# Kernel optimization log

Hardware: AMD Instinct MI355X
Metric: run time of the kernel (lower is better)

The kernel has to match this reference:

```python
import jax, jax.numpy as jnp
import numpy as np

GAIN_CAP = 0.99
EPS = 1e-4


def _clamp(v):
    # clamp_preserve_grad(v, 0.0, cap) == cap - relu(cap - relu(v))
    r = jax.nn.relu
    return GAIN_CAP - r(GAIN_CAP - r(v))


def _pos(p):
    return jax.nn.softplus(p) + EPS


def setup_inputs() -> dict:
    key = jax.random.key(0)
    ks = jax.random.split(key, 12)
    B, C, H, W, O, M = 4, 128, 256, 256, 16, 32
    return {
        "x": jax.random.normal(ks[0], (B, C, H, W), jnp.float32),
        "steer": jax.random.normal(ks[1], (B, O, H, W), jnp.float32),
        "modulation": jax.random.normal(ks[2], (B, M), jnp.float32),
        "r_center": 0.1 * jax.random.normal(ks[3], (C,), jnp.float32),
        "r_horizontal": 0.1 * jax.random.normal(ks[4], (C,), jnp.float32),
        "r_vertical": 0.1 * jax.random.normal(ks[5], (C,), jnp.float32),
        "r_diag": 0.1 * jax.random.normal(ks[6], (C,), jnp.float32),
        "gain_horizontal": 0.1 * jax.random.normal(ks[7], (C,), jnp.float32),
        "gain_vertical": 0.1 * jax.random.normal(ks[8], (C,), jnp.float32),
        "gain_diag": 0.1 * jax.random.normal(ks[9], (C,), jnp.float32),
        "steer_w": 0.1 * jax.random.normal(ks[10], (4, O), jnp.float32),  # 1x1 conv weight squeezed
        "mod_w": 0.1 * jax.random.normal(ks[11], (3, M), jnp.float32),    # Linear(M,3,bias=False)
    }


def reference(x, steer, modulation, r_center, r_horizontal, r_vertical, r_diag,
              gain_horizontal, gain_vertical, gain_diag, steer_w, mod_w):
    cview = lambda p: p[None, :, None, None]  # (1,C,1,1)
    center = x
    right = jnp.roll(x, -1, axis=-1)
    left = jnp.roll(x, 1, axis=-1)
    up = jnp.roll(x, 1, axis=-2)
    down = jnp.roll(x, -1, axis=-2)
    diag_ne = jnp.roll(x, (-1, -1), axis=(-2, -1))
    diag_sw = jnp.roll(x, (1, 1), axis=(-2, -1))
    diag_nw = jnp.roll(x, (1, -1), axis=(-2, -1))
    diag_se = jnp.roll(x, (-1, 1), axis=(-2, -1))

    r_c = cview(_pos(r_center))
    r_h = cview(_pos(r_horizontal))
    r_v = cview(_pos(r_vertical))
    r_d = cview(_pos(r_diag))

    flow_h = (right - center + (left - center)) / (r_c + r_h)
    flow_v = (up - center + (down - center)) / (r_c + r_v)
    flow_d = (diag_ne - center + (diag_sw - center) + (diag_nw - center) + (diag_se - center)) / (2.0 * (r_c + r_d))

    gh = jnp.tanh(cview(gain_horizontal))
    gv = jnp.tanh(cview(gain_vertical))
    gd = jnp.tanh(cview(gain_diag))

    # modulation gating: [B,3] -> [B,3,1,1]
    delta = jnp.tanh(modulation @ mod_w.T)[:, :, None, None]
    gh = _clamp(gh * (1.0 + 0.1 * delta[:, 0:1]))
    gv = _clamp(gv * (1.0 + 0.1 * delta[:, 1:2]))
    gd = _clamp(gd * (1.0 + 0.1 * delta[:, 2:3]))

    # steer gating: 1x1 conv (no bias) then tanh -> [B,4,H,W]
    steer_fields = jnp.tanh(jnp.einsum('bohw,po->bphw', steer, steer_w))
    gh = _clamp(gh * (1.0 + 0.2 * steer_fields[:, 0:1]))
    gv = _clamp(gv * (1.0 + 0.2 * steer_fields[:, 1:2]))
    gd = _clamp(gd * (1.0 + 0.2 * steer_fields[:, 2:3]))

    update = gh * flow_h + gv * flow_v + gd * flow_d
    return center + update
```

## Files before the change

kernel.cpp:

```cpp
#include <hip/hip_runtime.h>
#include <math.h>

#define GAIN_CAP 0.99f
#define EPSV 1e-4f

static constexpr int B = 4, C = 128, H = 256, W = 256, O = 16, M = 32;
static constexpr int HW = H * W;

static constexpr int SF_SZ = B * 3 * HW;
static constexpr int G_SZ  = B * C * 3;

__device__ __forceinline__ float softplusf(float x) {
    return log1pf(expf(-fabsf(x))) + fmaxf(x, 0.0f);
}
__device__ __forceinline__ float clampg(float v) {
    return fminf(fmaxf(v, 0.0f), GAIN_CAP);
}

__global__ void setup_kernel(const float* __restrict__ r_center,
                             const float* __restrict__ r_h,
                             const float* __restrict__ r_v,
                             const float* __restrict__ r_d,
                             const float* __restrict__ g_h,
                             const float* __restrict__ g_v,
                             const float* __restrict__ g_d,
                             const float* __restrict__ modulation,
                             const float* __restrict__ mod_w,
                             float* __restrict__ gains,
                             float* __restrict__ invd)
{
    int t = threadIdx.x;
    int b = t >> 7;
    int c = t & (C - 1);

    float rc = softplusf(r_center[c]) + EPSV;
    float dh = rc + softplusf(r_h[c]) + EPSV;
    float dv = rc + softplusf(r_v[c]) + EPSV;
    float dd = 2.0f * (rc + softplusf(r_d[c]) + EPSV);
    if (b == 0) {
        invd[c * 3 + 0] = 1.0f / dh;
        invd[c * 3 + 1] = 1.0f / dv;
        invd[c * 3 + 2] = 1.0f / dd;
    }

    float a0 = 0.f, a1 = 0.f, a2 = 0.f;
#pragma unroll
    for (int m = 0; m < M; ++m) {
        float mv = modulation[b * M + m];
        a0 += mv * mod_w[0 * M + m];
        a1 += mv * mod_w[1 * M + m];
        a2 += mv * mod_w[2 * M + m];
    }
    float d0 = tanhf(a0), d1 = tanhf(a1), d2 = tanhf(a2);

    gains[(b * C + c) * 3 + 0] = clampg(tanhf(g_h[c]) * (1.0f + 0.1f * d0));
    gains[(b * C + c) * 3 + 1] = clampg(tanhf(g_v[c]) * (1.0f + 0.1f * d1));
    gains[(b * C + c) * 3 + 2] = clampg(tanhf(g_d[c]) * (1.0f + 0.1f * d2));
}

__global__ void steer_kernel(const float* __restrict__ steer,
                             const float* __restrict__ steer_w,
                             float* __restrict__ sf)
{
    int idx = blockIdx.x * blockDim.x + threadIdx.x;
    int b  = idx >> 16;
    int hw = idx & (HW - 1);

    const float* sp = steer + (size_t)b * O * HW + hw;
    float a0 = 0.f, a1 = 0.f, a2 = 0.f;
#pragma unroll
    for (int o = 0; o < O; ++o) {
        float v = sp[(size_t)o * HW];
        a0 += v * steer_w[0 * O + o];
        a1 += v * steer_w[1 * O + o];
        a2 += v * steer_w[2 * O + o];
    }
    sf[(size_t)(b * 3 + 0) * HW + hw] = tanhf(a0);
    sf[(size_t)(b * 3 + 1) * HW + hw] = tanhf(a1);
    sf[(size_t)(b * 3 + 2) * HW + hw] = tanhf(a2);
}

__global__ void __launch_bounds__(256)
main_kernel(const float* __restrict__ x,
            const float* __restrict__ sf,
            const float* __restrict__ gains,
            const float* __restrict__ invd,
            float* __restrict__ out)
{
    int idx = blockIdx.x * 256 + threadIdx.x;
    int w  = idx & (W - 1);
    int h  = (idx >> 8) & (H - 1);
    int bc = idx >> 16;
    int c  = bc & (C - 1);
    int b  = bc >> 7;

    const float* plane = x + (size_t)bc * HW;
    int wp = (w + 1) & (W - 1), wm = (w - 1) & (W - 1);
    int hp = (h + 1) & (H - 1), hm = (h - 1) & (H - 1);
    const float* row_c = plane + h  * W;
    const float* row_u = plane + hm * W;
    const float* row_d = plane + hp * W;

    float center = row_c[w];
    float right  = row_c[wp], left = row_c[wm];
    float up     = row_u[w],  down = row_d[w];
    float ne = row_d[wp], sw = row_u[wm], nw = row_u[wp], se = row_d[wm];

    float fh = (right + left - 2.0f * center) * invd[c * 3 + 0];
    float fv = (up + down - 2.0f * center)    * invd[c * 3 + 1];
    float fd = (ne + sw + nw + se - 4.0f * center) * invd[c * 3 + 2];

    int hw = (h << 8) | w;
    float s0 = sf[(size_t)(b * 3 + 0) * HW + hw];
    float s1 = sf[(size_t)(b * 3 + 1) * HW + hw];
    float s2 = sf[(size_t)(b * 3 + 2) * HW + hw];

    float gh = clampg(gains[bc * 3 + 0] * (1.0f + 0.2f * s0));
    float gv = clampg(gains[bc * 3 + 1] * (1.0f + 0.2f * s1));
    float gd = clampg(gains[bc * 3 + 2] * (1.0f + 0.2f * s2));

    out[idx] = center + gh * fh + gv * fv + gd * fd;
}

extern "C" void kernel_launch(void* const* d_in, const int* in_sizes, int n_in,
                              void* d_out, int out_size, void* d_ws, size_t ws_size,
                              hipStream_t stream) {
    const float* x          = (const float*)d_in[0];
    const float* steer      = (const float*)d_in[1];
    const float* modulation = (const float*)d_in[2];
    const float* r_center   = (const float*)d_in[3];
    const float* r_horiz    = (const float*)d_in[4];
    const float* r_vert     = (const float*)d_in[5];
    const float* r_diag     = (const float*)d_in[6];
    const float* g_horiz    = (const float*)d_in[7];
    const float* g_vert     = (const float*)d_in[8];
    const float* g_diag     = (const float*)d_in[9];
    const float* steer_w    = (const float*)d_in[10];
    const float* mod_w      = (const float*)d_in[11];

    float* ws    = (float*)d_ws;
    float* sf    = ws;
    float* gains = ws + SF_SZ;
    float* invd  = gains + G_SZ;
    float* out   = (float*)d_out;

    setup_kernel<<<1, B * C, 0, stream>>>(r_center, r_horiz, r_vert, r_diag,
                                          g_horiz, g_vert, g_diag,
                                          modulation, mod_w, gains, invd);
    steer_kernel<<<(B * HW) / 256, 256, 0, stream>>>(steer, steer_w, sf);
    main_kernel<<<(B * C * HW) / 256, 256, 0, stream>>>(x, sf, gains, invd, out);
}
```

Baseline: 339.0 us.

## Row-streaming stencil with float4 loads, wave shuffles, and fused setup kernel

The main kernel now has each wavefront walk a strip of 16 rows of one plane. It loads each row once as float4 and keeps the up, center and down rows in registers, so vertical neighbours are reused across iterations. Horizontal neighbours come from cross-lane shuffles, and output goes out through non-temporal vector stores. The setup work is folded into the steer kernel, which is also vectorized to float4, removing one launch. The cost is fewer blocks, less parallelism and serial dependence along rows.

```diff
diff --git a/kernel.cpp b/kernel.cpp
--- a/kernel.cpp
+++ b/kernel.cpp
@@ -6,6 +6,8 @@
 
 static constexpr int B = 4, C = 128, H = 256, W = 256, O = 16, M = 32;
 static constexpr int HW = H * W;
+
+typedef float vfloat4 __attribute__((ext_vector_type(4)));
 
 static constexpr int SF_SZ = B * 3 * HW;
 static constexpr int G_SZ  = B * C * 3;
@@ -17,67 +19,64 @@
     return fminf(fmaxf(v, 0.0f), GAIN_CAP);
 }
 
-__global__ void setup_kernel(const float* __restrict__ r_center,
-                             const float* __restrict__ r_h,
-                             const float* __restrict__ r_v,
-                             const float* __restrict__ r_d,
-                             const float* __restrict__ g_h,
-                             const float* __restrict__ g_v,
-                             const float* __restrict__ g_d,
-                             const float* __restrict__ modulation,
-                             const float* __restrict__ mod_w,
-                             float* __restrict__ gains,
-                             float* __restrict__ invd)
+__global__ void __launch_bounds__(256)
+steer_kernel(const float* __restrict__ steer,
+             const float* __restrict__ steer_w,
+             const float* __restrict__ r_center,
+             const float* __restrict__ r_h,
+             const float* __restrict__ r_v,
+             const float* __restrict__ r_d,
+             const float* __restrict__ g_h,
+             const float* __restrict__ g_v,
+             const float* __restrict__ g_d,
+             const float* __restrict__ modulation,
+             const float* __restrict__ mod_w,
+             float* __restrict__ sf,
+             float* __restrict__ gains,
+             float* __restrict__ invd)
 {
-    int t = threadIdx.x;
-    int b = t >> 7;
-    int c = t & (C - 1);
-
-    float rc = softplusf(r_center[c]) + EPSV;
-    float dh = rc + softplusf(r_h[c]) + EPSV;
-    float dv = rc + softplusf(r_v[c]) + EPSV;
-    float dd = 2.0f * (rc + softplusf(r_d[c]) + EPSV);
-    if (b == 0) {
-        invd[c * 3 + 0] = 1.0f / dh;
-        invd[c * 3 + 1] = 1.0f / dv;
-        invd[c * 3 + 2] = 1.0f / dd;
+    if (blockIdx.x == 0 && threadIdx.x < C) {
+        int c = threadIdx.x;
+        float rc = softplusf(r_center[c]) + EPSV;
+        invd[c * 3 + 0] = 1.0f / (rc + softplusf(r_h[c]) + EPSV);
+        invd[c * 3 + 1] = 1.0f / (rc + softplusf(r_v[c]) + EPSV);
+        invd[c * 3 + 2] = 1.0f / (2.0f * (rc + softplusf(r_d[c]) + EPSV));
+        float th = tanhf(g_h[c]), tv = tanhf(g_v[c]), td = tanhf(g_d[c]);
+        for (int b = 0; b < B; ++b) {
+            float a0 = 0.f, a1 = 0.f, a2 = 0.f;
+#pragma unroll
+            for (int m = 0; m < M; ++m) {
+                float mv = modulation[b * M + m];
+                a0 += mv * mod_w[0 * M + m];
+                a1 += mv * mod_w[1 * M + m];
+                a2 += mv * mod_w[2 * M + m];
+            }
+            gains[(b * C + c) * 3 + 0] = clampg(th * (1.0f + 0.1f * tanhf(a0)));
+            gains[(b * C + c) * 3 + 1] = clampg(tv * (1.0f + 0.1f * tanhf(a1)));
+            gains[(b * C + c) * 3 + 2] = clampg(td * (1.0f + 0.1f * tanhf(a2)));
+        }
     }
 
-    float a0 = 0.f, a1 = 0.f, a2 = 0.f;
-#pragma unroll
-    for (int m = 0; m < M; ++m) {
-        float mv = modulation[b * M + m];
-        a0 += mv * mod_w[0 * M + m];
-        a1 += mv * mod_w[1 * M + m];
-        a2 += mv * mod_w[2 * M + m];
-    }
-    float d0 = tanhf(a0), d1 = tanhf(a1), d2 = tanhf(a2);
+    int idx = blockIdx.x * 256 + threadIdx.x;
+    int b   = idx >> 14;
+    int hw4 = idx & 16383;
+    const float4* sp = (const float4*)(steer + ((size_t)b * O << 16)) + hw4;
 
-    gains[(b * C + c) * 3 + 0] = clampg(tanhf(g_h[c]) * (1.0f + 0.1f * d0));
-    gains[(b * C + c) * 3 + 1] = clampg(tanhf(g_v[c]) * (1.0f + 0.1f * d1));
-    gains[(b * C + c) * 3 + 2] = clampg(tanhf(g_d[c]) * (1.0f + 0.1f * d2));
-}
-
-__global__ void steer_kernel(const float* __restrict__ steer,
-                             const float* __restrict__ steer_w,
-                             float* __restrict__ sf)
-{
-    int idx = blockIdx.x * blockDim.x + threadIdx.x;
-    int b  = idx >> 16;
-    int hw = idx & (HW - 1);
-
-    const float* sp = steer + (size_t)b * O * HW + hw;
-    float a0 = 0.f, a1 = 0.f, a2 = 0.f;
+    float4 a0 = {0,0,0,0}, a1 = {0,0,0,0}, a2 = {0,0,0,0};
 #pragma unroll
     for (int o = 0; o < O; ++o) {
-        float v = sp[(size_t)o * HW];
-        a0 += v * steer_w[0 * O + o];
-        a1 += v * steer_w[1 * O + o];
-        a2 += v * steer_w[2 * O + o];
+        float4 v = sp[(size_t)o << 14];
+        float w0 = steer_w[o], w1 = steer_w[O + o], w2 = steer_w[2 * O + o];
+        a0.x += v.x * w0; a0.y += v.y * w0; a0.z += v.z * w0; a0.w += v.w * w0;
+        a1.x += v.x * w1; a1.y += v.y * w1; a1.z += v.z * w1; a1.w += v.w * w1;
+        a2.x += v.x * w2; a2.y += v.y * w2; a2.z += v.z * w2; a2.w += v.w * w2;
     }
-    sf[(size_t)(b * 3 + 0) * HW + hw] = tanhf(a0);
-    sf[(size_t)(b * 3 + 1) * HW + hw] = tanhf(a1);
-    sf[(size_t)(b * 3 + 2) * HW + hw] = tanhf(a2);
+    float4* o0 = (float4*)(sf + ((size_t)(b * 3 + 0) << 16)) + hw4;
+    float4* o1 = (float4*)(sf + ((size_t)(b * 3 + 1) << 16)) + hw4;
+    float4* o2 = (float4*)(sf + ((size_t)(b * 3 + 2) << 16)) + hw4;
+    *o0 = make_float4(tanhf(a0.x), tanhf(a0.y), tanhf(a0.z), tanhf(a0.w));
+    *o1 = make_float4(tanhf(a1.x), tanhf(a1.y), tanhf(a1.z), tanhf(a1.w));
+    *o2 = make_float4(tanhf(a2.x), tanhf(a2.y), tanhf(a2.z), tanhf(a2.w));
 }
 
 __global__ void __launch_bounds__(256)
@@ -87,39 +86,70 @@
             const float* __restrict__ invd,
             float* __restrict__ out)
 {
-    int idx = blockIdx.x * 256 + threadIdx.x;
-    int w  = idx & (W - 1);
-    int h  = (idx >> 8) & (H - 1);
-    int bc = idx >> 16;
-    int c  = bc & (C - 1);
-    int b  = bc >> 7;
+    constexpr int RPW = 16;
+    int lane  = threadIdx.x & 63;
+    int wave  = threadIdx.x >> 6;
+    int strip = blockIdx.x & 3;
+    int bc    = blockIdx.x >> 2;
+    int c     = bc & (C - 1);
+    int b     = bc >> 7;
+    int h0    = strip * 64 + wave * RPW;
 
-    const float* plane = x + (size_t)bc * HW;
-    int wp = (w + 1) & (W - 1), wm = (w - 1) & (W - 1);
-    int hp = (h + 1) & (H - 1), hm = (h - 1) & (H - 1);
-    const float* row_c = plane + h  * W;
-    const float* row_u = plane + hm * W;
-    const float* row_d = plane + hp * W;
+    const float* plane = x + ((size_t)bc << 16);
+    const float* sfb0  = sf + ((size_t)(b * 3 + 0) << 16);
+    const float* sfb1  = sf + ((size_t)(b * 3 + 1) << 16);
+    const float* sfb2  = sf + ((size_t)(b * 3 + 2) << 16);
+    float*       outp  = out + ((size_t)bc << 16);
 
-    float center = row_c[w];
-    float right  = row_c[wp], left = row_c[wm];
-    float up     = row_u[w],  down = row_d[w];
-    float ne = row_d[wp], sw = row_u[wm], nw = row_u[wp], se = row_d[wm];
+    float ih  = invd[c * 3 + 0], iv = invd[c * 3 + 1], idg = invd[c * 3 + 2];
+    float g0  = gains[bc * 3 + 0], g1 = gains[bc * 3 + 1], g2 = gains[bc * 3 + 2];
 
-    float fh = (right + left - 2.0f * center) * invd[c * 3 + 0];
-    float fv = (up + down - 2.0f * center)    * invd[c * 3 + 1];
-    float fd = (ne + sw + nw + se - 4.0f * center) * invd[c * 3 + 2];
+    int lp = (lane + 1) & 63, lm = (lane - 1) & 63;
 
-    int hw = (h << 8) | w;
-    float s0 = sf[(size_t)(b * 3 + 0) * HW + hw];
-    float s1 = sf[(size_t)(b * 3 + 1) * HW + hw];
-    float s2 = sf[(size_t)(b * 3 + 2) * HW + hw];
+    float4 u4 = ((const float4*)(plane + (((h0 - 1) & 255) << 8)))[lane];
+    float4 c4 = ((const float4*)(plane + (h0 << 8)))[lane];
+    float uRe = __shfl(u4.x, lp), uLe = __shfl(u4.w, lm);
+    float cRe = __shfl(c4.x, lp), cLe = __shfl(c4.w, lm);
 
-    float gh = clampg(gains[bc * 3 + 0] * (1.0f + 0.2f * s0));
-    float gv = clampg(gains[bc * 3 + 1] * (1.0f + 0.2f * s1));
-    float gd = clampg(gains[bc * 3 + 2] * (1.0f + 0.2f * s2));
+    for (int r = 0; r < RPW; ++r) {
+        int h  = h0 + r;
+        int hd = (h + 1) & 255;
+        float4 d4 = ((const float4*)(plane + (hd << 8)))[lane];
+        float4 s0 = ((const float4*)(sfb0 + (h << 8)))[lane];
+        float4 s1 = ((const float4*)(sfb1 + (h << 8)))[lane];
+        float4 s2 = ((const float4*)(sfb2 + (h << 8)))[lane];
+        float dRe = __shfl(d4.x, lp), dLe = __shfl(d4.w, lm);
 
-    out[idx] = center + gh * fh + gv * fv + gd * fd;
+        float cA[4]  = {c4.x, c4.y, c4.z, c4.w};
+        float uA[4]  = {u4.x, u4.y, u4.z, u4.w};
+        float dA[4]  = {d4.x, d4.y, d4.z, d4.w};
+        float crA[4] = {c4.y, c4.z, c4.w, cRe};
+        float clA[4] = {cLe, c4.x, c4.y, c4.z};
+        float urA[4] = {u4.y, u4.z, u4.w, uRe};
+        float ulA[4] = {uLe, u4.x, u4.y, u4.z};
+        float drA[4] = {d4.y, d4.z, d4.w, dRe};
+        float dlA[4] = {dLe, d4.x, d4.y, d4.z};
+        float sA0[4] = {s0.x, s0.y, s0.z, s0.w};
+        float sA1[4] = {s1.x, s1.y, s1.z, s1.w};
+        float sA2[4] = {s2.x, s2.y, s2.z, s2.w};
+
+        float oA[4];
+#pragma unroll
+        for (int j = 0; j < 4; ++j) {
+            float fh = (crA[j] + clA[j] - 2.0f * cA[j]) * ih;
+            float fv = (uA[j] + dA[j] - 2.0f * cA[j]) * iv;
+            float fd = (drA[j] + dlA[j] + urA[j] + ulA[j] - 4.0f * cA[j]) * idg;
+            float gh = clampg(g0 * (1.0f + 0.2f * sA0[j]));
+            float gv = clampg(g1 * (1.0f + 0.2f * sA1[j]));
+            float gd = clampg(g2 * (1.0f + 0.2f * sA2[j]));
+            oA[j] = cA[j] + gh * fh + gv * fv + gd * fd;
+        }
+        vfloat4 ov = {oA[0], oA[1], oA[2], oA[3]};
+        __builtin_nontemporal_store(ov, (vfloat4*)(outp + (h << 8)) + lane);
+
+        u4 = c4; uRe = cRe; uLe = cLe;
+        c4 = d4; cRe = dRe; cLe = dLe;
+    }
 }
 
 extern "C" void kernel_launch(void* const* d_in, const int* in_sizes, int n_in,
@@ -144,9 +174,8 @@
     float* invd  = gains + G_SZ;
     float* out   = (float*)d_out;
 
-    setup_kernel<<<1, B * C, 0, stream>>>(r_center, r_horiz, r_vert, r_diag,
-                                          g_horiz, g_vert, g_diag,
-                                          modulation, mod_w, gains, invd);
-    steer_kernel<<<(B * HW) / 256, 256, 0, stream>>>(steer, steer_w, sf);
-    main_kernel<<<(B * C * HW) / 256, 256, 0, stream>>>(x, sf, gains, invd, out);
+    steer_kernel<<<(B * HW / 4) / 256, 256, 0, stream>>>(
+        steer, steer_w, r_center, r_horiz, r_vert, r_diag,
+        g_horiz, g_vert, g_diag, modulation, mod_w, sf, gains, invd);
+    main_kernel<<<B * C * 4, 256, 0, stream>>>(x, sf, gains, invd, out);
 }
```

New measurement: 284.2 us. 1.19x faster.
